# Kernel tuning notes

Measured on AMD Instinct MI355X. Metric: run time of the kernel, lower is better.

The kernel has to match this reference:

```python
import jax, jax.numpy as jnp
import numpy as np

EMBED_DIM = 1024
HEADS = 16
HEAD_DIM = EMBED_DIM // HEADS
SEQ = 2048
N_BATCH = 4


def setup_inputs() -> dict:
    key = jax.random.key(0)
    ks = jax.random.split(key, 9)
    s = 1.0 / np.sqrt(HEAD_DIM)
    so = 1.0 / np.sqrt(EMBED_DIM)
    return {
        "values": jax.random.normal(ks[0], (SEQ, N_BATCH, EMBED_DIM), jnp.float32),
        "keys": jax.random.normal(ks[1], (SEQ, N_BATCH, EMBED_DIM), jnp.float32),
        "queries": jax.random.normal(ks[2], (SEQ, N_BATCH, EMBED_DIM), jnp.float32),
        "src_mask": jax.random.randint(ks[3], (N_BATCH, 1, 1, SEQ), 0, 2, jnp.int32),
        "Wv": jax.random.uniform(ks[4], (HEAD_DIM, HEAD_DIM), jnp.float32, -s, s),
        "Wk": jax.random.uniform(ks[5], (HEAD_DIM, HEAD_DIM), jnp.float32, -s, s),
        "Wq": jax.random.uniform(ks[6], (HEAD_DIM, HEAD_DIM), jnp.float32, -s, s),
        "Wo": jax.random.uniform(ks[7], (EMBED_DIM, EMBED_DIM), jnp.float32, -so, so),
        "bo": jax.random.uniform(ks[8], (EMBED_DIM,), jnp.float32, -so, so),
    }


def reference(values, keys, queries, src_mask, Wv, Wk, Wq, Wo, bo):
    N = queries.shape[1]
    Lv, Lk, Lq = values.shape[0], keys.shape[0], queries.shape[0]
    # Faithful to the original (buggy) reshape of (L, N, E) -> (N, L, H, D)
    v = values.reshape(N, Lv, HEADS, HEAD_DIM) @ Wv.T
    k = keys.reshape(N, Lk, HEADS, HEAD_DIM) @ Wk.T
    q = queries.reshape(N, Lq, HEADS, HEAD_DIM) @ Wq.T
    energy = jnp.einsum("nqhd,nkhd->nhqk", q, k)  # (N, H, Q, K)
    energy = jnp.where(src_mask == 0, jnp.float32(-1e20), energy)
    attn = jax.nn.softmax(energy / jnp.sqrt(jnp.float32(EMBED_DIM)), axis=3)
    out = jnp.einsum("nhql,nlhd->nqhd", attn, v).reshape(Lq, N, EMBED_DIM)
    return out @ Wo.T + bo
```

## Files before the change

### kernel.cpp

```cpp
#include <hip/hip_runtime.h>
#include <hip/hip_bf16.h>
#include <stdint.h>
#include <string.h>

#define EMBED 1024
#define HEADS 16
#define HD    64
#define SEQ   2048
#define NB    4
#define ROWS  (SEQ * NB)
#define NH    (NB * HEADS)

typedef __attribute__((ext_vector_type(8)))  short short8;
typedef __attribute__((ext_vector_type(4)))  float f32x4;
typedef __attribute__((ext_vector_type(16))) float f32x16;
typedef __attribute__((ext_vector_type(4)))  unsigned short u16x4;

#define MFMA16(a, b, c) __builtin_amdgcn_mfma_f32_16x16x32_bf16((a), (b), (c), 0, 0, 0)
#define MFMA32(a, b, c) __builtin_amdgcn_mfma_f32_32x32x16_bf16((a), (b), (c), 0, 0, 0)

__device__ inline unsigned short f2b(float f) {
    unsigned u = __builtin_bit_cast(unsigned, f);
    u += 0x7fffu + ((u >> 16) & 1u);
    return (unsigned short)(u >> 16);
}

__device__ inline unsigned pk2(float a, float b) {
    __hip_bfloat162 h = __float22bfloat162_rn(make_float2(a, b));
    unsigned r;
    __builtin_memcpy(&r, &h, 4);
    return r;
}

#define EXP2(x) __builtin_amdgcn_exp2f(x)

__device__ inline short8 ld8(const unsigned short* p) {
    return *reinterpret_cast<const short8*>(p);
}

__global__ __launch_bounds__(256) void cvt_bf16_kernel(const float* __restrict__ in,
                                                       unsigned short* __restrict__ out,
                                                       int nelem) {
    int i = (blockIdx.x * 256 + threadIdx.x) * 4;
    if (i + 3 < nelem) {
        float4 v = *reinterpret_cast<const float4*>(in + i);
        u16x4 o;
        o[0] = f2b(v.x); o[1] = f2b(v.y); o[2] = f2b(v.z); o[3] = f2b(v.w);
        *reinterpret_cast<u16x4*>(out + i) = o;
    }
}

__global__ __launch_bounds__(64) void maskbits_kernel(const int* __restrict__ mask,
                                                      unsigned* __restrict__ mb) {
    int w = blockIdx.x * 64 + threadIdx.x;
    unsigned v = 0;
#pragma unroll
    for (int j = 0; j < 32; ++j)
        v |= (mask[w * 32 + j] != 0 ? 1u : 0u) << j;
    mb[w] = v;
}

__global__ __launch_bounds__(64) void proj_kernel(const float* __restrict__ X,
                                                  const float* __restrict__ W,
                                                  unsigned short* __restrict__ out) {
    const int lane = threadIdx.x;
    const int lo = lane & 15, hi = lane >> 4;
    const int r0 = blockIdx.x * 16;
    const int h  = blockIdx.y;

    short8 a[2];
#pragma unroll
    for (int s = 0; s < 2; ++s) {
        const float4* src = reinterpret_cast<const float4*>(
            X + (size_t)(r0 + lo) * EMBED + h * HD + s * 32 + hi * 8);
        float4 v0 = src[0], v1 = src[1];
        short8 t;
        t[0] = (short)f2b(v0.x); t[1] = (short)f2b(v0.y);
        t[2] = (short)f2b(v0.z); t[3] = (short)f2b(v0.w);
        t[4] = (short)f2b(v1.x); t[5] = (short)f2b(v1.y);
        t[6] = (short)f2b(v1.z); t[7] = (short)f2b(v1.w);
        a[s] = t;
    }
    short8 b[4][2];
#pragma unroll
    for (int u = 0; u < 4; ++u)
#pragma unroll
        for (int s = 0; s < 2; ++s) {
            const float4* src = reinterpret_cast<const float4*>(
                W + (size_t)(16 * u + lo) * HD + s * 32 + hi * 8);
            float4 v0 = src[0], v1 = src[1];
            short8 t;
            t[0] = (short)f2b(v0.x); t[1] = (short)f2b(v0.y);
            t[2] = (short)f2b(v0.z); t[3] = (short)f2b(v0.w);
            t[4] = (short)f2b(v1.x); t[5] = (short)f2b(v1.y);
            t[6] = (short)f2b(v1.z); t[7] = (short)f2b(v1.w);
            b[u][s] = t;
        }

    f32x4 acc[4] = {};
#pragma unroll
    for (int u = 0; u < 4; ++u)
#pragma unroll
        for (int s = 0; s < 2; ++s)
            acc[u] = MFMA16(a[s], b[u][s], acc[u]);

    const int n  = r0 >> 11;
    const int l0 = r0 & (SEQ - 1);
    const size_t nh = (size_t)(n * HEADS + h);
#pragma unroll
    for (int u = 0; u < 4; ++u)
#pragma unroll
        for (int r = 0; r < 4; ++r)
            out[nh * (SEQ * HD) + (size_t)(l0 + hi * 4 + r) * HD + 16 * u + lo] =
                f2b(acc[u][r]);
}

__global__ __launch_bounds__(256) void projv_kernel(const float* __restrict__ X,
                                                    const float* __restrict__ W,
                                                    unsigned short* __restrict__ out) {
    const int tid = threadIdx.x;
    const int w = tid >> 6, lane = tid & 63;
    const int lo = lane & 15, hi = lane >> 4;
    const int r0 = blockIdx.x * 64;
    const int rw = r0 + w * 16;
    const int h  = blockIdx.y;

    __shared__ unsigned short T[64 * 73];

    short8 a[2];
#pragma unroll
    for (int s = 0; s < 2; ++s) {
        const float4* src = reinterpret_cast<const float4*>(
            X + (size_t)(rw + lo) * EMBED + h * HD + s * 32 + hi * 8);
        float4 v0 = src[0], v1 = src[1];
        short8 t;
        t[0] = (short)f2b(v0.x); t[1] = (short)f2b(v0.y);
        t[2] = (short)f2b(v0.z); t[3] = (short)f2b(v0.w);
        t[4] = (short)f2b(v1.x); t[5] = (short)f2b(v1.y);
        t[6] = (short)f2b(v1.z); t[7] = (short)f2b(v1.w);
        a[s] = t;
    }
    short8 b[4][2];
#pragma unroll
    for (int u = 0; u < 4; ++u)
#pragma unroll
        for (int s = 0; s < 2; ++s) {
            const float4* src = reinterpret_cast<const float4*>(
                W + (size_t)(16 * u + lo) * HD + s * 32 + hi * 8);
            float4 v0 = src[0], v1 = src[1];
            short8 t;
            t[0] = (short)f2b(v0.x); t[1] = (short)f2b(v0.y);
            t[2] = (short)f2b(v0.z); t[3] = (short)f2b(v0.w);
            t[4] = (short)f2b(v1.x); t[5] = (short)f2b(v1.y);
            t[6] = (short)f2b(v1.z); t[7] = (short)f2b(v1.w);
            b[u][s] = t;
        }

    f32x4 acc[4] = {};
#pragma unroll
    for (int u = 0; u < 4; ++u)
#pragma unroll
        for (int s = 0; s < 2; ++s)
            acc[u] = MFMA16(a[s], b[u][s], acc[u]);

#pragma unroll
    for (int u = 0; u < 4; ++u)
#pragma unroll
        for (int r = 0; r < 4; ++r)
            T[(w * 16 + hi * 4 + r) * 73 + 16 * u + lo] = f2b(acc[u][r]);
    __syncthreads();

    const int d = tid >> 2, lc = (tid & 3) * 16;
    const int n = r0 >> 11, l0 = r0 & (SEQ - 1);
    union { unsigned short s[16]; uint4 v[2]; } pk;
#pragma unroll
    for (int j = 0; j < 16; ++j) pk.s[j] = T[(lc + j) * 73 + d];
    unsigned short* dst = out + (size_t)(n * HEADS + h) * (HD * SEQ)
                              + (size_t)d * SEQ + l0 + lc;
    *reinterpret_cast<uint4*>(dst)     = pk.v[0];
    *reinterpret_cast<uint4*>(dst + 8) = pk.v[1];
}

#define KST 72
#define VST 40

__global__ __launch_bounds__(128, 2) void attn_kernel(const unsigned short* __restrict__ Qb,
                                                      const unsigned short* __restrict__ Kb,
                                                      const unsigned short* __restrict__ Vt,
                                                      const unsigned* __restrict__ mbits,
                                                      unsigned short* __restrict__ Aout) {
    const int tid  = threadIdx.x;
    const int w    = tid >> 6;
    const int lane = tid & 63;
    const int lo = lane & 31, hi = lane >> 5;
    const int nhidx = blockIdx.y;
    const int n = nhidx >> 4, h = nhidx & 15;
    const int q0 = blockIdx.x * 128 + w * 64;

    const unsigned short* Qp = Qb + (size_t)nhidx * SEQ * HD;
    const unsigned short* Kp = Kb + (size_t)nhidx * SEQ * HD;
    const unsigned short* Vp = Vt + (size_t)nhidx * HD * SEQ;
    const unsigned* mb = mbits + n * (SEQ / 32);

    __shared__ __align__(16) unsigned short Klds[2][32 * KST];
    __shared__ __align__(16) unsigned short Vlds[2][64 * VST];

    const int kr = (tid * 2) >> 3, kb0 = ((tid * 2) & 7) * 8;
    const int vr = (tid * 2) >> 2, vb0 = ((tid * 2) & 3) * 8;

    uint4 stK0, stK1, stV0, stV1;
#define LOADSTAGE(KB_)                                                        \
    {                                                                         \
        const unsigned short* kp_ = Kp + (size_t)((KB_) + kr) * HD + kb0;     \
        const unsigned short* vp_ = Vp + (size_t)vr * SEQ + (KB_) + vb0;      \
        stK0 = *reinterpret_cast<const uint4*>(kp_);                          \
        stK1 = *reinterpret_cast<const uint4*>(kp_ + 8);                      \
        stV0 = *reinterpret_cast<const uint4*>(vp_);                          \
        stV1 = *reinterpret_cast<const uint4*>(vp_ + 8);                      \
    }
#define WRITESTAGE(BUF)                                                       \
    {                                                                         \
        *reinterpret_cast<uint4*>(&Klds[BUF][kr * KST + kb0])     = stK0;     \
        *reinterpret_cast<uint4*>(&Klds[BUF][kr * KST + kb0 + 8]) = stK1;     \
        uint4 pv0, pv1;                                                       \
        pv0.x = stV0.x; pv0.y = stV0.y; pv0.z = stV1.z; pv0.w = stV1.w;       \
        pv1.x = stV0.z; pv1.y = stV0.w; pv1.z = stV1.x; pv1.w = stV1.y;       \
        *reinterpret_cast<uint4*>(&Vlds[BUF][vr * VST + vb0])     = pv0;      \
        *reinterpret_cast<uint4*>(&Vlds[BUF][vr * VST + vb0 + 8]) = pv1;      \
    }

    short8 qfA[4], qfB[4];
#pragma unroll
    for (int s = 0; s < 4; ++s) {
        qfA[s] = ld8(Qp + (size_t)(q0 + lo) * HD + s * 16 + hi * 8);
        qfB[s] = ld8(Qp + (size_t)(q0 + 32 + lo) * HD + s * 16 + hi * 8);
    }

    f32x16 o0A = {}, o1A = {}, o0B = {}, o1B = {};
    float lsumA = 0.0f, lsumB = 0.0f;

    const float KS    = 0.045084220027780106f;
    const float M0    = 8.0f;
    const float TMASK = -4.5e18f;

    LOADSTAGE(0)

    int cur = 0;
    for (int kt = 0; kt < SEQ / 32; ++kt) {
        WRITESTAGE(cur)
        if (kt + 1 < SEQ / 32) LOADSTAGE((kt + 1) * 32)
        __syncthreads();

        const unsigned short* Kl = Klds[cur];
        const unsigned short* Vl = Vlds[cur];

        f32x16 saA = {}, saB = {};
#pragma unroll
        for (int s = 0; s < 4; ++s) {
            short8 kf = *reinterpret_cast<const short8*>(Kl + lo * KST + s * 16 + hi * 8);
            saA = MFMA32(kf, qfA[s], saA);
            saB = MFMA32(kf, qfB[s], saB);
        }

        short8 vf[2][2];
#pragma unroll
        for (int dt = 0; dt < 2; ++dt)
#pragma unroll
            for (int s = 0; s < 2; ++s)
                vf[dt][s] = *reinterpret_cast<const short8*>(
                    Vl + (32 * dt + lo) * VST + s * 16 + hi * 8);

        unsigned mw = mb[kt] >> (4 * hi);
        float pA[16], pB[16];
#pragma unroll
        for (int r = 0; r < 16; ++r) {
            const int bp = (r & 3) + 8 * (r >> 2);
            const bool keep = (mw >> bp) & 1u;
            float ta = fmaf(saA[r], KS, -M0);
            float tb = fmaf(saB[r], KS, -M0);
            float ea = EXP2(keep ? ta : TMASK);
            float eb = EXP2(keep ? tb : TMASK);
            pA[r] = ea; lsumA += ea;
            pB[r] = eb; lsumB += eb;
        }

#define PACK_PB(P, PB_)                                                       \
        {                                                                     \
            unsigned W0[4], W1[4];                                            \
            _Pragma("unroll") for (int g = 0; g < 4; ++g) {                   \
                W0[g] = pk2(P[4 * g],     P[4 * g + 1]);                      \
                W1[g] = pk2(P[4 * g + 2], P[4 * g + 3]);                      \
            }                                                                 \
            _Pragma("unroll") for (int s2 = 0; s2 < 2; ++s2) {                \
                unsigned sw0 = (unsigned)__shfl_xor((int)W0[2 * s2 + 1], 32); \
                unsigned sw1 = (unsigned)__shfl_xor((int)W1[2 * s2 + 1], 32); \
                union { short8 s8; unsigned u[4]; } uu;                       \
                uu.u[0] = W0[2 * s2]; uu.u[1] = W1[2 * s2];                   \
                uu.u[2] = sw0;        uu.u[3] = sw1;                          \
                (PB_)[s2] = uu.s8;                                            \
            }                                                                 \
        }
        short8 pbA[2], pbB[2];
        PACK_PB(pA, pbA)
        PACK_PB(pB, pbB)
#undef PACK_PB

#pragma unroll
        for (int s = 0; s < 2; ++s) {
            o0A = MFMA32(vf[0][s], pbA[s], o0A);
            o1A = MFMA32(vf[1][s], pbA[s], o1A);
            o0B = MFMA32(vf[0][s], pbB[s], o0B);
            o1B = MFMA32(vf[1][s], pbB[s], o1B);
        }

        __syncthreads();
        cur ^= 1;
    }

    float lA = lsumA + __shfl_xor(lsumA, 32);
    float lB = lsumB + __shfl_xor(lsumB, 32);

    float invA = 1.0f / lA;
    float invB = 1.0f / lB;
    const size_t rbA = (size_t)(n * SEQ + q0 + lo) * EMBED + h * HD;
    const size_t rbB = (size_t)(n * SEQ + q0 + 32 + lo) * EMBED + h * HD;
#pragma unroll
    for (int r = 0; r < 16; ++r) {
        int dl = (r & 3) + 8 * (r >> 2) + 4 * hi;
        Aout[rbA + dl]      = f2b(o0A[r] * invA);
        Aout[rbA + 32 + dl] = f2b(o1A[r] * invA);
        Aout[rbB + dl]      = f2b(o0B[r] * invB);
        Aout[rbB + 32 + dl] = f2b(o1B[r] * invB);
    }
#undef LOADSTAGE
#undef WRITESTAGE
}

#define OST 40
__global__ __launch_bounds__(256, 2) void outproj_kernel(const unsigned short* __restrict__ A,
                                                         const unsigned short* __restrict__ Wob,
                                                         const float* __restrict__ bo,
                                                         float* __restrict__ Y) {
    const int tid  = threadIdx.x;
    const int w    = tid >> 6;
    const int lane = tid & 63;
    const int lo = lane & 15, hi = lane >> 4;
    const int r0 = blockIdx.x * 128;
    const int c0 = blockIdx.y * 128;

    __shared__ __align__(16) unsigned short Al[128 * OST];
    __shared__ __align__(16) unsigned short Bl[128 * OST];

    const int srow = tid >> 2, scb = (tid & 3) * 8;
    uint4 sA0, sA1, sB0, sB1;
#define OLOAD(K_)                                                             \
    {                                                                         \
        sA0 = *reinterpret_cast<const uint4*>(A + (size_t)(r0 + srow) * EMBED + (K_) + scb);        \
        sA1 = *reinterpret_cast<const uint4*>(A + (size_t)(r0 + 64 + srow) * EMBED + (K_) + scb);   \
        sB0 = *reinterpret_cast<const uint4*>(Wob + (size_t)(c0 + srow) * EMBED + (K_) + scb);      \
        sB1 = *reinterpret_cast<const uint4*>(Wob + (size_t)(c0 + 64 + srow) * EMBED + (K_) + scb); \
    }
#define OWRITE()                                                              \
    {                                                                         \
        *reinterpret_cast<uint4*>(&Al[srow * OST + scb])        = sA0;        \
        *reinterpret_cast<uint4*>(&Al[(64 + srow) * OST + scb]) = sA1;        \
        *reinterpret_cast<uint4*>(&Bl[srow * OST + scb])        = sB0;        \
        *reinterpret_cast<uint4*>(&Bl[(64 + srow) * OST + scb]) = sB1;        \
    }

    f32x4 acc[2][8] = {};
    OLOAD(0)
    for (int kt = 0; kt < EMBED / 32; ++kt) {
        OWRITE()
        if (kt + 1 < EMBED / 32) OLOAD((kt + 1) * 32)
        __syncthreads();

        short8 a0 = ld8(&Al[(w * 32 + lo) * OST + hi * 8]);
        short8 a1 = ld8(&Al[(w * 32 + 16 + lo) * OST + hi * 8]);
#pragma unroll
        for (int u = 0; u < 8; ++u) {
            short8 b = ld8(&Bl[(u * 16 + lo) * OST + hi * 8]);
            acc[0][u] = MFMA16(a0, b, acc[0][u]);
            acc[1][u] = MFMA16(a1, b, acc[1][u]);
        }
        __syncthreads();
    }

#pragma unroll
    for (int mi = 0; mi < 2; ++mi)
#pragma unroll
        for (int u = 0; u < 8; ++u) {
            int e = c0 + u * 16 + lo;
            float bv = bo[e];
#pragma unroll
            for (int r = 0; r < 4; ++r)
                Y[(size_t)(r0 + w * 32 + mi * 16 + hi * 4 + r) * EMBED + e] =
                    acc[mi][u][r] + bv;
        }
#undef OLOAD
#undef OWRITE
}

extern "C" void kernel_launch(void* const* d_in, const int* in_sizes, int n_in,
                              void* d_out, int out_size, void* d_ws, size_t ws_size,
                              hipStream_t stream) {
    const float* values  = (const float*)d_in[0];
    const float* keys    = (const float*)d_in[1];
    const float* queries = (const float*)d_in[2];
    const int*   mask    = (const int*)d_in[3];
    const float* Wv = (const float*)d_in[4];
    const float* Wk = (const float*)d_in[5];
    const float* Wq = (const float*)d_in[6];
    const float* Wo = (const float*)d_in[7];
    const float* bo = (const float*)d_in[8];
    float* Y = (float*)d_out;

    const size_t QKV     = (size_t)NH * SEQ * HD * sizeof(unsigned short);
    const size_t ABYTES  = (size_t)ROWS * EMBED * sizeof(unsigned short);
    const size_t WOBYTES = (size_t)EMBED * EMBED * sizeof(unsigned short);
    const size_t MBYTES  = (size_t)NB * (SEQ / 32) * sizeof(unsigned);
    if (ws_size < 3 * QKV + ABYTES + WOBYTES + MBYTES) return;

    char* ws = (char*)d_ws;
    unsigned short* Qb  = (unsigned short*)(ws);
    unsigned short* Kb  = (unsigned short*)(ws + QKV);
    unsigned short* Vt  = (unsigned short*)(ws + 2 * QKV);
    unsigned short* Ab  = (unsigned short*)(ws + 3 * QKV);
    unsigned short* Wob = (unsigned short*)(ws + 3 * QKV + ABYTES);
    unsigned*       Mb  = (unsigned*)(ws + 3 * QKV + ABYTES + WOBYTES);

    cvt_bf16_kernel<<<dim3(EMBED * EMBED / (256 * 4)), 256, 0, stream>>>(Wo, Wob, EMBED * EMBED);
    maskbits_kernel<<<dim3(4), 64, 0, stream>>>(mask, Mb);
    proj_kernel<<<dim3(ROWS / 16, HEADS), 64, 0, stream>>>(queries, Wq, Qb);
    proj_kernel<<<dim3(ROWS / 16, HEADS), 64, 0, stream>>>(keys,    Wk, Kb);
    projv_kernel<<<dim3(ROWS / 64, HEADS), 256, 0, stream>>>(values, Wv, Vt);
    attn_kernel<<<dim3(SEQ / 128, NH), 128, 0, stream>>>(Qb, Kb, Vt, Mb, Ab);
    outproj_kernel<<<dim3(ROWS / 128, EMBED / 128), 256, 0, stream>>>(Ab, Wob, bo, Y);
}
```

Before: 202.3 us.

## Split attention key range across two block halves and merge partial outputs

```diff
diff --git a/kernel.cpp b/kernel.cpp
--- a/kernel.cpp
+++ b/kernel.cpp
@@ -183,14 +183,19 @@
 
 #define KST 72
 #define VST 40
-
-__global__ __launch_bounds__(128, 2) void attn_kernel(const unsigned short* __restrict__ Qb,
+#define KHE (2 * 32 * KST)
+#define VHE (2 * 64 * VST)
+#define SHE (2 * KHE + 2 * VHE)
+
+__global__ __launch_bounds__(256, 4) void attn_kernel(const unsigned short* __restrict__ Qb,
                                                       const unsigned short* __restrict__ Kb,
                                                       const unsigned short* __restrict__ Vt,
                                                       const unsigned* __restrict__ mbits,
                                                       unsigned short* __restrict__ Aout) {
     const int tid  = threadIdx.x;
-    const int w    = tid >> 6;
+    const int half = tid >> 7;
+    const int t    = tid & 127;
+    const int w    = (tid >> 6) & 1;
     const int lane = tid & 63;
     const int lo = lane & 31, hi = lane >> 5;
     const int nhidx = blockIdx.y;
@@ -202,11 +207,12 @@
     const unsigned short* Vp = Vt + (size_t)nhidx * HD * SEQ;
     const unsigned* mb = mbits + n * (SEQ / 32);
 
-    __shared__ __align__(16) unsigned short Klds[2][32 * KST];
-    __shared__ __align__(16) unsigned short Vlds[2][64 * VST];
-
-    const int kr = (tid * 2) >> 3, kb0 = ((tid * 2) & 7) * 8;
-    const int vr = (tid * 2) >> 2, vb0 = ((tid * 2) & 3) * 8;
+    __shared__ __align__(16) unsigned short SH[SHE];
+    unsigned short* Kbase = SH + half * KHE;
+    unsigned short* Vbase = SH + 2 * KHE + half * VHE;
+
+    const int kr = (t * 2) >> 3, kb0 = ((t * 2) & 7) * 8;
+    const int vr = (t * 2) >> 2, vb0 = ((t * 2) & 3) * 8;
 
     uint4 stK0, stK1, stV0, stV1;
 #define LOADSTAGE(KB_)                                                        \
@@ -220,13 +226,15 @@
     }
 #define WRITESTAGE(BUF)                                                       \
     {                                                                         \
-        *reinterpret_cast<uint4*>(&Klds[BUF][kr * KST + kb0])     = stK0;     \
-        *reinterpret_cast<uint4*>(&Klds[BUF][kr * KST + kb0 + 8]) = stK1;     \
+        unsigned short* kd_ = Kbase + (BUF) * (32 * KST);                     \
+        unsigned short* vd_ = Vbase + (BUF) * (64 * VST);                     \
+        *reinterpret_cast<uint4*>(kd_ + kr * KST + kb0)     = stK0;           \
+        *reinterpret_cast<uint4*>(kd_ + kr * KST + kb0 + 8) = stK1;           \
         uint4 pv0, pv1;                                                       \
         pv0.x = stV0.x; pv0.y = stV0.y; pv0.z = stV1.z; pv0.w = stV1.w;       \
         pv1.x = stV0.z; pv1.y = stV0.w; pv1.z = stV1.x; pv1.w = stV1.y;       \
-        *reinterpret_cast<uint4*>(&Vlds[BUF][vr * VST + vb0])     = pv0;      \
-        *reinterpret_cast<uint4*>(&Vlds[BUF][vr * VST + vb0 + 8]) = pv1;      \
+        *reinterpret_cast<uint4*>(vd_ + vr * VST + vb0)     = pv0;            \
+        *reinterpret_cast<uint4*>(vd_ + vr * VST + vb0 + 8) = pv1;            \
     }
 
     short8 qfA[4], qfB[4];
@@ -243,16 +251,16 @@
     const float M0    = 8.0f;
     const float TMASK = -4.5e18f;
 
-    LOADSTAGE(0)
+    LOADSTAGE(half * 1024)
 
     int cur = 0;
-    for (int kt = 0; kt < SEQ / 32; ++kt) {
+    for (int kt = 0; kt < 32; ++kt) {
         WRITESTAGE(cur)
-        if (kt + 1 < SEQ / 32) LOADSTAGE((kt + 1) * 32)
+        if (kt + 1 < 32) LOADSTAGE(half * 1024 + (kt + 1) * 32)
         __syncthreads();
 
-        const unsigned short* Kl = Klds[cur];
-        const unsigned short* Vl = Vlds[cur];
+        const unsigned short* Kl = Kbase + cur * (32 * KST);
+        const unsigned short* Vl = Vbase + cur * (64 * VST);
 
         f32x16 saA = {}, saB = {};
 #pragma unroll
@@ -270,7 +278,7 @@
                 vf[dt][s] = *reinterpret_cast<const short8*>(
                     Vl + (32 * dt + lo) * VST + s * 16 + hi * 8);
 
-        unsigned mw = mb[kt] >> (4 * hi);
+        unsigned mw = mb[half * 32 + kt] >> (4 * hi);
         float pA[16], pB[16];
 #pragma unroll
         for (int r = 0; r < 16; ++r) {
@@ -317,20 +325,44 @@
         cur ^= 1;
     }
 
-    float lA = lsumA + __shfl_xor(lsumA, 32);
-    float lB = lsumB + __shfl_xor(lsumB, 32);
-
-    float invA = 1.0f / lA;
-    float invB = 1.0f / lB;
-    const size_t rbA = (size_t)(n * SEQ + q0 + lo) * EMBED + h * HD;
-    const size_t rbB = (size_t)(n * SEQ + q0 + 32 + lo) * EMBED + h * HD;
-#pragma unroll
-    for (int r = 0; r < 16; ++r) {
-        int dl = (r & 3) + 8 * (r >> 2) + 4 * hi;
-        Aout[rbA + dl]      = f2b(o0A[r] * invA);
-        Aout[rbA + 32 + dl] = f2b(o1A[r] * invA);
-        Aout[rbB + dl]      = f2b(o0B[r] * invB);
-        Aout[rbB + 32 + dl] = f2b(o1B[r] * invB);
+    float* M = reinterpret_cast<float*>(SH);
+    if (half == 1) {
+#pragma unroll
+        for (int r = 0; r < 16; ++r) {
+            M[t + 128 * r]        = o0A[r];
+            M[t + 128 * (16 + r)] = o1A[r];
+            M[t + 128 * (32 + r)] = o0B[r];
+            M[t + 128 * (48 + r)] = o1B[r];
+        }
+        M[t + 128 * 64] = lsumA;
+        M[t + 128 * 65] = lsumB;
+    }
+    __syncthreads();
+    if (half == 0) {
+#pragma unroll
+        for (int r = 0; r < 16; ++r) {
+            o0A[r] += M[t + 128 * r];
+            o1A[r] += M[t + 128 * (16 + r)];
+            o0B[r] += M[t + 128 * (32 + r)];
+            o1B[r] += M[t + 128 * (48 + r)];
+        }
+        lsumA += M[t + 128 * 64];
+        lsumB += M[t + 128 * 65];
+
+        float lA = lsumA + __shfl_xor(lsumA, 32);
+        float lB = lsumB + __shfl_xor(lsumB, 32);
+        float invA = 1.0f / lA;
+        float invB = 1.0f / lB;
+        const size_t rbA = (size_t)(n * SEQ + q0 + lo) * EMBED + h * HD;
+        const size_t rbB = (size_t)(n * SEQ + q0 + 32 + lo) * EMBED + h * HD;
+#pragma unroll
+        for (int r = 0; r < 16; ++r) {
+            int dl = (r & 3) + 8 * (r >> 2) + 4 * hi;
+            Aout[rbA + dl]      = f2b(o0A[r] * invA);
+            Aout[rbA + 32 + dl] = f2b(o1A[r] * invA);
+            Aout[rbB + dl]      = f2b(o0B[r] * invB);
+            Aout[rbB + 32 + dl] = f2b(o1B[r] * invB);
+        }
     }
 #undef LOADSTAGE
 #undef WRITESTAGE
@@ -434,6 +466,6 @@
     proj_kernel<<<dim3(ROWS / 16, HEADS), 64, 0, stream>>>(queries, Wq, Qb);
     proj_kernel<<<dim3(ROWS / 16, HEADS), 64, 0, stream>>>(keys,    Wk, Kb);
     projv_kernel<<<dim3(ROWS / 64, HEADS), 256, 0, stream>>>(values, Wv, Vt);
-    attn_kernel<<<dim3(SEQ / 128, NH), 128, 0, stream>>>(Qb, Kb, Vt, Mb, Ab);
+    attn_kernel<<<dim3(SEQ / 128, NH), 256, 0, stream>>>(Qb, Kb, Vt, Mb, Ab);
     outproj_kernel<<<dim3(ROWS / 128, EMBED / 128), 256, 0, stream>>>(Ab, Wob, bo, Y);
 }
```

After: 546.4 us. +170.1%, slower.
